# Kernel optimization log

Measured on AMD Instinct MI355X. Metric: run time of the kernel, lower is better.

## Reference

```python
import jax, jax.numpy as jnp
import numpy as np

NEG_INF = 1e20  # matches INF in the torch source
EPS = 1e-12     # F.normalize default eps
THRESHOLD = 0.1  # config.graph_learn_epsilon_label2label


def setup_inputs() -> dict:
    key = jax.random.key(0)
    k1, k2, k3, k4, k5 = jax.random.split(key, 5)
    L, E, E_PT, H = 2048, 512, 300, 16
    return {
        "label_embedding": jax.random.normal(k1, (L, E), dtype=jnp.float32),
        "pretrained_label_embedding": jax.random.normal(k2, (L, E_PT), dtype=jnp.float32),
        "W_pt": jax.random.normal(k3, (H, E_PT), dtype=jnp.float32) * 0.1,
        "W_gcn0": jax.random.normal(k4, (E, E), dtype=jnp.float32) * (1.0 / np.sqrt(E)),
        "W_gcn1": jax.random.normal(k5, (E, E), dtype=jnp.float32) * (1.0 / np.sqrt(E)),
    }


def _weighted_cosine(input_pt, W_pt):
    # W_pt: [H, E_pt]; input_pt: [L, E_pt]
    w2 = W_pt ** 2                                  # [H, E_pt]
    h = input_pt[None, :, :] * w2[:, None, :]       # [H, L, E_pt]
    norm = jnp.linalg.norm(h, axis=-1, keepdims=True)
    h_norm = h / jnp.maximum(norm, EPS)             # F.normalize(p=2, dim=-1)
    # mean over heads of per-head cosine similarity: [L, L]
    scores = jnp.einsum("hle,hme->hlm", h_norm, h_norm).mean(axis=0)
    return scores


def reference(label_embedding, pretrained_label_embedding, W_pt, W_gcn0, W_gcn1):
    # 1) metric-based graph structure learning
    scores_cosine = _weighted_cosine(pretrained_label_embedding, W_pt)
    scores = jnp.where(scores_cosine >= THRESHOLD, scores_cosine, -NEG_INF)
    adj = jax.nn.softmax(scores, axis=-1)           # [L, L]

    # 2) 2-layer GCN message passing (bias=None, batch_norm=False, eval-mode dropout)
    x = jax.nn.relu(adj @ (label_embedding @ W_gcn0))
    x = jax.nn.relu(adj @ (x @ W_gcn1))
    return x
```

## Files before the change

kernel.cpp:

```cpp
#include <hip/hip_runtime.h>
#include <hip/hip_bf16.h>


typedef __attribute__((ext_vector_type(8))) short bf16x8;
typedef __attribute__((ext_vector_type(4))) float f32x4;
typedef __attribute__((ext_vector_type(4))) int i32x4;

#define L_DIM 2048
#define EPT 300
#define H_DIM 16
#define KDIM 4800
#define WINDOW 1.5e-3f

__global__ __launch_bounds__(256) void prep_kernel(const float* __restrict__ xpt,
                                                   const float* __restrict__ Wpt,
                                                   const float* __restrict__ label,
                                                   const float* __restrict__ W0,
                                                   const float* __restrict__ W1,
                                                   signed char* __restrict__ Y,
                                                   float* __restrict__ rnorms,
                                                   float* __restrict__ inv_s,
                                                   __hip_bfloat16* __restrict__ Lbf,
                                                   __hip_bfloat16* __restrict__ W0t,
                                                   __hip_bfloat16* __restrict__ W1t) {
  __shared__ float redmax[4];
  __shared__ float tile[32][33];
  const int b = blockIdx.x;
  const int tid = threadIdx.x;
  if (b < 2048) {
    const int i = b;
    const int lane = tid & 63;
    const int w = tid >> 6;
    const float* x = xpt + i * EPT;
    float y[4][5];
    float wmax = 0.f;
#pragma unroll
    for (int hh = 0; hh < 4; ++hh) {
      const int h = w * 4 + hh;
      const float* wp = Wpt + h * EPT;
      float ss = 0.f;
#pragma unroll
      for (int t = 0; t < 5; ++t) {
        int e = lane + 64 * t;
        float val = 0.f;
        if (e < EPT) {
          float we = wp[e];
          val = x[e] * we * we;
        }
        y[hh][t] = val;
        ss += val * val;
      }
#pragma unroll
      for (int o = 32; o >= 1; o >>= 1) ss += __shfl_xor(ss, o, 64);
      float n = fmaxf(sqrtf(ss), 1e-12f);
      if (lane == 0) rnorms[i * H_DIM + h] = 1.0f / n;
      float scale = 0.25f / n;
#pragma unroll
      for (int t = 0; t < 5; ++t) {
        y[hh][t] *= scale;
        wmax = fmaxf(wmax, fabsf(y[hh][t]));
      }
    }
#pragma unroll
    for (int o = 32; o >= 1; o >>= 1) wmax = fmaxf(wmax, __shfl_xor(wmax, o, 64));
    if (lane == 0) redmax[w] = wmax;
    __syncthreads();
    float rowmax = fmaxf(fmaxf(redmax[0], redmax[1]), fmaxf(redmax[2], redmax[3]));
    rowmax = fmaxf(rowmax, 1e-12f);
    const float qs = 127.0f / rowmax;
    if (tid == 0) inv_s[i] = rowmax * (1.0f / 127.0f);
#pragma unroll
    for (int hh = 0; hh < 4; ++hh) {
      const int h = w * 4 + hh;
#pragma unroll
      for (int t = 0; t < 5; ++t) {
        int e = lane + 64 * t;
        if (e < EPT) {
          int qv = __float2int_rn(y[hh][t] * qs);
          qv = max(-127, min(127, qv));
          Y[(size_t)i * KDIM + h * EPT + e] = (signed char)qv;
        }
      }
    }
    return;
  }
  if (b < 6144) {
    int i = (b - 2048) * 256 + tid;
    Lbf[i] = __float2bfloat16(label[i]);
    return;
  }
  int local = b - 6144;
  const bool first = local < 256;
  const float* src = first ? W0 : W1;
  __hip_bfloat16* dst = first ? W0t : W1t;
  int rem = local & 255;
  int c0 = (rem & 15) * 32, r0 = (rem >> 4) * 32;
  int tx = tid & 31, ty = tid >> 5;
  for (int i2 = ty; i2 < 32; i2 += 8) tile[i2][tx] = src[(size_t)(r0 + i2) * 512 + c0 + tx];
  __syncthreads();
  for (int i2 = ty; i2 < 32; i2 += 8)
    dst[(size_t)(c0 + i2) * 512 + r0 + tx] = __float2bfloat16(tile[tx][i2]);
}

__global__ __launch_bounds__(256) void gram_i8(const signed char* __restrict__ Y,
                                               float* __restrict__ S,
                                               const float* __restrict__ inv_s,
                                               const __hip_bfloat16* __restrict__ W0t,
                                               const __hip_bfloat16* __restrict__ Lbf,
                                               __hip_bfloat16* __restrict__ T0t) {
  __shared__ __attribute__((aligned(16))) char smem[32768];
  const int id = blockIdx.x;
  const int bx = (id & 7) | (((id >> 3) & 3) << 3);
  const int by = id >> 5;
  const int row0 = by * 64, col0 = bx * 64;
  const int tid = threadIdx.x;
  const int lane = tid & 63;
  const int wn = tid >> 6;
  const int r = lane & 15, q = lane >> 4;

  if (col0 + 64 <= row0) {
    const int d = (by * (by - 1)) / 2 + bx;
    if (d >= 256) return;
    const int row0r = (d >> 5) * 64;
    const int col0r = (d & 31) * 64;
    __hip_bfloat16* Asb = (__hip_bfloat16*)smem;
    __hip_bfloat16* Bsb = (__hip_bfloat16*)(smem + 16384);
    const int srow8 = tid >> 3;
    const int schunk8 = (tid & 7) ^ (srow8 & 7);
    f32x4 racc[4];
#pragma unroll
    for (int t = 0; t < 4; ++t) {
      f32x4 z = {0.f, 0.f, 0.f, 0.f};
      racc[t] = z;
    }
#define RSTAGE(bufi, k0)                                                                      \
  {                                                                                           \
    _Pragma("unroll") for (int it = 0; it < 2; ++it) {                                        \
      __builtin_amdgcn_global_load_lds(                                                       \
          (const __attribute__((address_space(1))) void*)(W0t + (size_t)(row0r + it * 32 + srow8) * 512 + \
                                                          (k0) + schunk8 * 8),                \
          (__attribute__((address_space(3))) void*)(Asb + (bufi)*4096 + (it * 256 + tid) * 8), 16, 0, 0); \
    }                                                                                         \
    _Pragma("unroll") for (int it = 0; it < 2; ++it) {                                        \
      __builtin_amdgcn_global_load_lds(                                                       \
          (const __attribute__((address_space(1))) void*)(Lbf + (size_t)(col0r + it * 32 + srow8) * 512 + \
                                                          (k0) + schunk8 * 8),                \
          (__attribute__((address_space(3))) void*)(Bsb + (bufi)*4096 + (it * 256 + tid) * 8), 16, 0, 0); \
    }                                                                                         \
  }
    RSTAGE(0, 0)
    for (int k = 0; k < 8; ++k) {
      __syncthreads();
      if (k + 1 < 8) RSTAGE((k + 1) & 1, (k + 1) * 64)
      const __hip_bfloat16* as = Asb + (k & 1) * 4096;
      const __hip_bfloat16* bs = Bsb + (k & 1) * 4096;
#pragma unroll
      for (int kk = 0; kk < 2; ++kk) {
        const int ch = ((kk * 4 + q) ^ (r & 7)) * 8;
        bf16x8 af[4];
#pragma unroll
        for (int t = 0; t < 4; ++t) af[t] = *(const bf16x8*)(as + (t * 16 + r) * 64 + ch);
        bf16x8 bfr = *(const bf16x8*)(bs + (wn * 16 + r) * 64 + ch);
#pragma unroll
        for (int t = 0; t < 4; ++t)
          racc[t] = __builtin_amdgcn_mfma_f32_16x16x32_bf16(af[t], bfr, racc[t], 0, 0, 0);
      }
    }
#undef RSTAGE
    const int gcr = col0r + wn * 16 + r;
#pragma unroll
    for (int t = 0; t < 4; ++t) {
      int gr0 = row0r + t * 16 + q * 4;
#pragma unroll
      for (int p = 0; p < 4; ++p)
        T0t[(size_t)(gr0 + p) * 2048 + gcr] = __float2bfloat16(racc[t][p]);
    }
    return;
  }

  const bool do_mirror = (col0 > row0);
  signed char* As = (signed char*)smem;
  signed char* Bs = (signed char*)(smem + 16384);
  const int srow = tid >> 2;
  const int sc = (tid & 3) ^ ((srow >> 2) & 3);

  i32x4 acc[4];
#pragma unroll
  for (int t = 0; t < 4; ++t) {
    i32x4 z = {0, 0, 0, 0};
    acc[t] = z;
  }
  const int niter = KDIM / 64;

#define STAGEI(bufi, k0)                                                                       \
  {                                                                                            \
    __builtin_amdgcn_global_load_lds(                                                          \
        (const __attribute__((address_space(1))) void*)(Y + (size_t)(row0 + srow) * KDIM +     \
                                                        (k0) + sc * 16),                       \
        (__attribute__((address_space(3))) void*)(As + (bufi)*4096 + tid * 16), 16, 0, 0);     \
    __builtin_amdgcn_global_load_lds(                                                          \
        (const __attribute__((address_space(1))) void*)(Y + (size_t)(col0 + srow) * KDIM +     \
                                                        (k0) + sc * 16),                       \
        (__attribute__((address_space(3))) void*)(Bs + (bufi)*4096 + tid * 16), 16, 0, 0);     \
  }

  auto compute = [&](int bufi) {
    const signed char* as = As + bufi * 4096;
    const signed char* bs = Bs + bufi * 4096;
    const int ch = (q ^ ((r >> 2) & 3)) * 16;
    i32x4 bfrag = *(const i32x4*)(bs + (wn * 16 + r) * 64 + ch);
#pragma unroll
    for (int t = 0; t < 4; ++t) {
      i32x4 afrag = *(const i32x4*)(as + (t * 16 + r) * 64 + ch);
      acc[t] = __builtin_amdgcn_mfma_i32_16x16x64_i8(afrag, bfrag, acc[t], 0, 0, 0);
    }
  };

  STAGEI(0, 0)
  STAGEI(1, 64)
  STAGEI(2, 128)
  for (int k = 0; k < niter - 3; ++k) {
    asm volatile("s_waitcnt vmcnt(4)" ::: "memory");
    __builtin_amdgcn_s_barrier();
    __builtin_amdgcn_sched_barrier(0);
    STAGEI((k + 3) & 3, (k + 3) * 64)
    compute(k & 3);
  }
  asm volatile("s_waitcnt vmcnt(4)" ::: "memory");
  __builtin_amdgcn_s_barrier();
  __builtin_amdgcn_sched_barrier(0);
  compute((niter - 3) & 3);
  asm volatile("s_waitcnt vmcnt(2)" ::: "memory");
  __builtin_amdgcn_s_barrier();
  __builtin_amdgcn_sched_barrier(0);
  compute((niter - 2) & 3);
  asm volatile("s_waitcnt vmcnt(0)" ::: "memory");
  __builtin_amdgcn_s_barrier();
  __builtin_amdgcn_sched_barrier(0);
  compute((niter - 1) & 3);
#undef STAGEI
  const int gc = col0 + wn * 16 + r;
  const float sj = inv_s[gc];
#pragma unroll
  for (int t = 0; t < 4; ++t) {
    int gr0 = row0 + t * 16 + q * 4;
#pragma unroll
    for (int p = 0; p < 4; ++p) {
      float vv = (float)acc[t][p] * (inv_s[gr0 + p] * sj);
      S[(size_t)(gr0 + p) * L_DIM + gc] = vv;
      if (do_mirror) S[(size_t)gc * L_DIM + (gr0 + p)] = vv;
    }
  }
}

template <int BM, int BN, bool RELU, bool OUT_BF16>
__global__ __launch_bounds__(256) void gemm_bt(const __hip_bfloat16* __restrict__ A,
                                               const __hip_bfloat16* __restrict__ B,
                                               void* __restrict__ C0v,
                                               int M, int N, int K) {
  constexpr int WMG = BM / 64;
  constexpr int WNG = 4 / WMG;
  constexpr int NC = BN / (16 * WNG);
  const int row0 = blockIdx.y * BM, col0 = blockIdx.x * BN;
  __shared__ __attribute__((aligned(16))) __hip_bfloat16 As[2][BM * 64];
  __shared__ __attribute__((aligned(16))) __hip_bfloat16 Bs[2][BN * 64];
  const int tid = threadIdx.x;
  const int lane = tid & 63;
  const int wave = tid >> 6;
  const int wm = wave / WNG, wn = wave % WNG;
  const int r = lane & 15, q = lane >> 4;
  const int srow = tid >> 3;
  const int schunk = (tid & 7) ^ (srow & 7);

  f32x4 acc[4][NC];
#pragma unroll
  for (int a = 0; a < 4; ++a)
#pragma unroll
    for (int b = 0; b < NC; ++b) {
      f32x4 z = {0.f, 0.f, 0.f, 0.f};
      acc[a][b] = z;
    }

  const int niter = K >> 6;

#define STAGE(bufi, k0)                                                                       \
  {                                                                                           \
    _Pragma("unroll") for (int it = 0; it < BM / 32; ++it) {                                  \
      __builtin_amdgcn_global_load_lds(                                                       \
          (const __attribute__((address_space(1))) void*)(A + (size_t)(row0 + it * 32 + srow) * K + \
                                                          (k0) + schunk * 8),                 \
          (__attribute__((address_space(3))) void*)(&As[bufi][(it * 256 + tid) * 8]), 16, 0, 0); \
    }                                                                                         \
    _Pragma("unroll") for (int it = 0; it < BN / 32; ++it) {                                  \
      __builtin_amdgcn_global_load_lds(                                                       \
          (const __attribute__((address_space(1))) void*)(B + (size_t)(col0 + it * 32 + srow) * K + \
                                                          (k0) + schunk * 8),                 \
          (__attribute__((address_space(3))) void*)(&Bs[bufi][(it * 256 + tid) * 8]), 16, 0, 0); \
    }                                                                                         \
  }

  STAGE(0, 0)
  for (int k = 0; k < niter; ++k) {
    __syncthreads();
    if (k + 1 < niter) STAGE((k + 1) & 1, (k + 1) << 6)
    const __hip_bfloat16* as = As[k & 1];
    const __hip_bfloat16* bs = Bs[k & 1];
#pragma unroll
    for (int kk = 0; kk < 2; ++kk) {
      const int ch = ((kk * 4 + q) ^ (r & 7)) * 8;
      bf16x8 af[4], bfr[NC];
#pragma unroll
      for (int t = 0; t < 4; ++t)
        af[t] = *(const bf16x8*)(as + (wm * 64 + t * 16 + r) * 64 + ch);
#pragma unroll
      for (int c = 0; c < NC; ++c)
        bfr[c] = *(const bf16x8*)(bs + (wn * 16 * NC + c * 16 + r) * 64 + ch);
#pragma unroll
      for (int tm = 0; tm < 4; ++tm)
#pragma unroll
        for (int tn = 0; tn < NC; ++tn)
          acc[tm][tn] = __builtin_amdgcn_mfma_f32_16x16x32_bf16(af[tm], bfr[tn], acc[tm][tn], 0, 0, 0);
    }
  }
#undef STAGE
#pragma unroll
  for (int tm = 0; tm < 4; ++tm) {
    int gr0 = row0 + wm * 64 + tm * 16 + q * 4;
#pragma unroll
    for (int tn = 0; tn < NC; ++tn) {
      int gc = col0 + wn * 16 * NC + tn * 16 + r;
#pragma unroll
      for (int p = 0; p < 4; ++p) {
        float vv = acc[tm][tn][p];
        if (RELU) vv = fmaxf(vv, 0.f);
        if (OUT_BF16) {
          ((__hip_bfloat16*)C0v)[(size_t)(gr0 + p) * N + gc] = __float2bfloat16(vv);
        } else {
          ((float*)C0v)[(size_t)(gr0 + p) * N + gc] = vv;
        }
      }
    }
  }
}

template <bool OUT_BF16>
__global__ __launch_bounds__(512) void gemm_adj_fused(const __hip_bfloat16* __restrict__ A,
                                                      const __hip_bfloat16* __restrict__ B,
                                                      void* __restrict__ C0v) {
  constexpr int K = 2048, N = 512;
  __shared__ __attribute__((aligned(16))) __hip_bfloat16 sm[4][2][4096];
  const int tid = threadIdx.x;
  const int grp = tid >> 8;
  const int gtid = tid & 255;
  const int lane = tid & 63;
  const int wn = (tid >> 6) & 3;
  const int r = lane & 15, q = lane >> 4;
  const int srow = gtid >> 3;
  const int schunk = (gtid & 7) ^ (srow & 7);
  const int row0 = blockIdx.y * 64, col0 = blockIdx.x * 64;
  const int kbeg = grp * 1024;
  __hip_bfloat16* As = &sm[grp * 2 + 0][0][0];
  __hip_bfloat16* Bs = &sm[grp * 2 + 1][0][0];

  f32x4 acc[4];
#pragma unroll
  for (int t = 0; t < 4; ++t) {
    f32x4 z = {0.f, 0.f, 0.f, 0.f};
    acc[t] = z;
  }

#define FSTAGE(bufi, k0)                                                                      \
  {                                                                                           \
    _Pragma("unroll") for (int it = 0; it < 2; ++it) {                                        \
      __builtin_amdgcn_global_load_lds(                                                       \
          (const __attribute__((address_space(1))) void*)(A + (size_t)(row0 + it * 32 + srow) * K + \
                                                          (k0) + schunk * 8),                 \
          (__attribute__((address_space(3))) void*)(As + (bufi)*4096 + (it * 256 + gtid) * 8), 16, 0, 0); \
    }                                                                                         \
    _Pragma("unroll") for (int it = 0; it < 2; ++it) {                                        \
      __builtin_amdgcn_global_load_lds(                                                       \
          (const __attribute__((address_space(1))) void*)(B + (size_t)(col0 + it * 32 + srow) * K + \
                                                          (k0) + schunk * 8),                 \
          (__attribute__((address_space(3))) void*)(Bs + (bufi)*4096 + (it * 256 + gtid) * 8), 16, 0, 0); \
    }                                                                                         \
  }

  FSTAGE(0, kbeg)
  for (int k = 0; k < 16; ++k) {
    __syncthreads();
    if (k + 1 < 16) FSTAGE((k + 1) & 1, kbeg + ((k + 1) << 6))
    const __hip_bfloat16* as = As + (k & 1) * 4096;
    const __hip_bfloat16* bs = Bs + (k & 1) * 4096;
#pragma unroll
    for (int kk = 0; kk < 2; ++kk) {
      const int ch = ((kk * 4 + q) ^ (r & 7)) * 8;
      bf16x8 af[4];
#pragma unroll
      for (int t = 0; t < 4; ++t) af[t] = *(const bf16x8*)(as + (t * 16 + r) * 64 + ch);
      bf16x8 bfr = *(const bf16x8*)(bs + (wn * 16 + r) * 64 + ch);
#pragma unroll
      for (int t = 0; t < 4; ++t)
        acc[t] = __builtin_amdgcn_mfma_f32_16x16x32_bf16(af[t], bfr, acc[t], 0, 0, 0);
    }
  }
#undef FSTAGE
  __syncthreads();
  float* F = (float*)&sm[2][0][0];
  if (grp == 1) {
#pragma unroll
    for (int tm = 0; tm < 4; ++tm)
#pragma unroll
      for (int p = 0; p < 4; ++p) F[gtid * 16 + tm * 4 + p] = acc[tm][p];
  }
  __syncthreads();
  if (grp == 0) {
#pragma unroll
    for (int tm = 0; tm < 4; ++tm) {
      int gr0 = row0 + tm * 16 + q * 4;
      int gc = col0 + wn * 16 + r;
#pragma unroll
      for (int p = 0; p < 4; ++p) {
        float vv = fmaxf(acc[tm][p] + F[gtid * 16 + tm * 4 + p], 0.f);
        if (OUT_BF16) {
          ((__hip_bfloat16*)C0v)[(size_t)(gr0 + p) * N + gc] = __float2bfloat16(vv);
        } else {
          ((float*)C0v)[(size_t)(gr0 + p) * N + gc] = vv;
        }
      }
    }
  }
}

__global__ __launch_bounds__(256) void post_kernel(const float* __restrict__ S,
                                                   __hip_bfloat16* __restrict__ adj,
                                                   const float* __restrict__ xpt,
                                                   const float* __restrict__ Wpt,
                                                   const float* __restrict__ rnorms) {
  __shared__ float rowv[L_DIM];
  __shared__ int lq[1024];
  __shared__ int lcount;
  __shared__ float red[4];
  const int b = blockIdx.x;
  const int tid = threadIdx.x;
  if (tid == 0) lcount = 0;
  __syncthreads();
  const float* s = S + (size_t)b * L_DIM;
  for (int j0 = tid * 4; j0 < L_DIM; j0 += 1024) {
    float4 v = *(const float4*)(s + j0);
    *(float4*)(&rowv[j0]) = v;
    float vv[4] = {v.x, v.y, v.z, v.w};
#pragma unroll
    for (int u = 0; u < 4; ++u) {
      if (fabsf(vv[u] - 0.1f) < WINDOW) {
        int p = atomicAdd(&lcount, 1);
        if (p < 1024) lq[p] = j0 + u;
      }
    }
  }
  __syncthreads();
  const int n = min(lcount, 1024);
  if (n > 0) {
    const int lane = tid & 63;
    const int wave = tid >> 6;
    float xiv[5];
    float w4i[H_DIM][5];
    {
      const float* xi = xpt + b * EPT;
#pragma unroll
      for (int t = 0; t < 5; ++t) {
        int idx = lane + 64 * t;
        xiv[t] = idx < EPT ? xi[idx] : 0.f;
      }
#pragma unroll
      for (int h = 0; h < H_DIM; ++h) {
        float rni = rnorms[b * H_DIM + h];
#pragma unroll
        for (int t = 0; t < 5; ++t) {
          int idx = lane + 64 * t;
          float w = idx < EPT ? Wpt[h * EPT + idx] : 0.f;
          float w2 = w * w;
          w4i[h][t] = w2 * w2 * rni;
        }
      }
    }
    for (int k = wave; k < n; k += 4) {
      int j = lq[k];
      const float* xj = xpt + j * EPT;
      float pre[5];
#pragma unroll
      for (int t = 0; t < 5; ++t) {
        int idx = lane + 64 * t;
        pre[t] = idx < EPT ? xiv[t] * xj[idx] : 0.f;
      }
      float accv = 0.f;
#pragma unroll
      for (int h = 0; h < H_DIM; ++h) {
        float ph = 0.f;
#pragma unroll
        for (int t = 0; t < 5; ++t) ph += pre[t] * w4i[h][t];
        accv += ph * rnorms[j * H_DIM + h];
      }
#pragma unroll
      for (int o = 32; o >= 1; o >>= 1) accv += __shfl_xor(accv, o, 64);
      if (lane == 0) rowv[j] = accv * (1.f / 16.f);
    }
    __syncthreads();
  }
  float m = -1e30f;
  for (int j = tid; j < L_DIM; j += 256) {
    float v = rowv[j];
    if (v >= 0.1f && v > m) m = v;
  }
#pragma unroll
  for (int o = 32; o >= 1; o >>= 1) m = fmaxf(m, __shfl_xor(m, o, 64));
  if ((tid & 63) == 0) red[tid >> 6] = m;
  __syncthreads();
  m = fmaxf(fmaxf(red[0], red[1]), fmaxf(red[2], red[3]));
  float sum = 0.f;
  for (int j = tid; j < L_DIM; j += 256) {
    float v = rowv[j];
    if (v >= 0.1f) sum += __expf(v - m);
  }
#pragma unroll
  for (int o = 32; o >= 1; o >>= 1) sum += __shfl_xor(sum, o, 64);
  __syncthreads();
  if ((tid & 63) == 0) red[tid >> 6] = sum;
  __syncthreads();
  sum = red[0] + red[1] + red[2] + red[3];
  float inv = 1.f / sum;
  for (int j = tid; j < L_DIM; j += 256) {
    float v = rowv[j];
    float a = (v >= 0.1f) ? __expf(v - m) * inv : 0.f;
    adj[(size_t)b * L_DIM + j] = __float2bfloat16(a);
  }
}

extern "C" void kernel_launch(void* const* d_in, const int* in_sizes, int n_in, void* d_out,
                              int out_size, void* d_ws, size_t ws_size, hipStream_t stream) {
  const float* label = (const float*)d_in[0];
  const float* xpt = (const float*)d_in[1];
  const float* Wpt = (const float*)d_in[2];
  const float* W0 = (const float*)d_in[3];
  const float* W1 = (const float*)d_in[4];
  float* out = (float*)d_out;

  char* ws = (char*)d_ws;
  signed char* Y = (signed char*)ws;
  float* S = (float*)(ws + 19660800);
  float* rnorms = (float*)(ws + 36438016);
  float* inv_s = (float*)(ws + 44957696);
  __hip_bfloat16* Lbf = (__hip_bfloat16*)(ws + 44965888);
  __hip_bfloat16* adj = (__hip_bfloat16*)ws;
  __hip_bfloat16* W0t = (__hip_bfloat16*)(ws + 10485760);
  __hip_bfloat16* W1t = (__hip_bfloat16*)(ws + 11010048);
  __hip_bfloat16* T0t = (__hip_bfloat16*)(ws + 11534336);
  __hip_bfloat16* X1 = (__hip_bfloat16*)(ws + 13631488);
  __hip_bfloat16* T1t = (__hip_bfloat16*)(ws + 15728640);

  prep_kernel<<<6656, 256, 0, stream>>>(xpt, Wpt, label, W0, W1, Y, rnorms, inv_s, Lbf, W0t, W1t);
  gram_i8<<<1024, 256, 0, stream>>>(Y, S, inv_s, W0t, Lbf, T0t);
  post_kernel<<<2048, 256, 0, stream>>>(S, adj, xpt, Wpt, rnorms);
  gemm_adj_fused<true><<<dim3(8, 32), 512, 0, stream>>>(adj, T0t, X1);
  gemm_bt<64, 64, false, true><<<dim3(32, 8), 256, 0, stream>>>(W1t, X1, T1t, 512, 2048, 512);
  gemm_adj_fused<false><<<dim3(8, 32), 512, 0, stream>>>(adj, T1t, out);
}
```

Before: 180.9 us.

## Switch int8 Gram GEMM to 128-wide K tiles with double buffering

The int8 similarity GEMM main loop now stages 128-byte K slices per iteration in two LDS buffers instead of 64-byte slices in a four-deep ring. It uses an 8-way XOR swizzle and a 64-wide tail step for the leftover K. The aim is to halve the number of barrier and loop iterations and to issue two MFMAs per fragment load. In exchange the prefetch depth drops from three stages to one, and __syncthreads waits for all loads each iteration, which may expose memory latency.

```diff
diff --git a/kernel.cpp b/kernel.cpp
--- a/kernel.cpp
+++ b/kernel.cpp
@@ -181,8 +181,6 @@
   const bool do_mirror = (col0 > row0);
   signed char* As = (signed char*)smem;
   signed char* Bs = (signed char*)(smem + 16384);
-  const int srow = tid >> 2;
-  const int sc = (tid & 3) ^ ((srow >> 2) & 3);
 
   i32x4 acc[4];
 #pragma unroll
@@ -190,55 +188,79 @@
     i32x4 z = {0, 0, 0, 0};
     acc[t] = z;
   }
-  const int niter = KDIM / 64;
-
-#define STAGEI(bufi, k0)                                                                       \
+  constexpr int NF = 37;
+
+#define STAGE128(bufi, k0)                                                                     \
   {                                                                                            \
+    _Pragma("unroll") for (int it = 0; it < 2; ++it) {                                         \
+      const int idx = it * 256 + tid;                                                          \
+      const int srw = idx >> 3;                                                                \
+      const int scc = (idx & 7) ^ (srw & 7);                                                   \
+      __builtin_amdgcn_global_load_lds(                                                        \
+          (const __attribute__((address_space(1))) void*)(Y + (size_t)(row0 + srw) * KDIM +    \
+                                                          (k0) + scc * 16),                    \
+          (__attribute__((address_space(3))) void*)(As + (bufi)*8192 + idx * 16), 16, 0, 0);   \
+    }                                                                                          \
+    _Pragma("unroll") for (int it = 0; it < 2; ++it) {                                         \
+      const int idx = it * 256 + tid;                                                          \
+      const int srw = idx >> 3;                                                                \
+      const int scc = (idx & 7) ^ (srw & 7);                                                   \
+      __builtin_amdgcn_global_load_lds(                                                        \
+          (const __attribute__((address_space(1))) void*)(Y + (size_t)(col0 + srw) * KDIM +    \
+                                                          (k0) + scc * 16),                    \
+          (__attribute__((address_space(3))) void*)(Bs + (bufi)*8192 + idx * 16), 16, 0, 0);   \
+    }                                                                                          \
+  }
+
+#define STAGETAIL(bufi, k0)                                                                    \
+  {                                                                                            \
+    const int srw = tid >> 2;                                                                  \
+    const int scc = (tid & 3) ^ ((srw >> 2) & 3);                                              \
     __builtin_amdgcn_global_load_lds(                                                          \
-        (const __attribute__((address_space(1))) void*)(Y + (size_t)(row0 + srow) * KDIM +     \
-                                                        (k0) + sc * 16),                       \
-        (__attribute__((address_space(3))) void*)(As + (bufi)*4096 + tid * 16), 16, 0, 0);     \
+        (const __attribute__((address_space(1))) void*)(Y + (size_t)(row0 + srw) * KDIM +      \
+                                                        (k0) + scc * 16),                      \
+        (__attribute__((address_space(3))) void*)(As + (bufi)*8192 + tid * 16), 16, 0, 0);     \
     __builtin_amdgcn_global_load_lds(                                                          \
-        (const __attribute__((address_space(1))) void*)(Y + (size_t)(col0 + srow) * KDIM +     \
-                                                        (k0) + sc * 16),                       \
-        (__attribute__((address_space(3))) void*)(Bs + (bufi)*4096 + tid * 16), 16, 0, 0);     \
-  }
-
-  auto compute = [&](int bufi) {
-    const signed char* as = As + bufi * 4096;
-    const signed char* bs = Bs + bufi * 4096;
-    const int ch = (q ^ ((r >> 2) & 3)) * 16;
-    i32x4 bfrag = *(const i32x4*)(bs + (wn * 16 + r) * 64 + ch);
-#pragma unroll
-    for (int t = 0; t < 4; ++t) {
-      i32x4 afrag = *(const i32x4*)(as + (t * 16 + r) * 64 + ch);
-      acc[t] = __builtin_amdgcn_mfma_i32_16x16x64_i8(afrag, bfrag, acc[t], 0, 0, 0);
-    }
-  };
-
-  STAGEI(0, 0)
-  STAGEI(1, 64)
-  STAGEI(2, 128)
-  for (int k = 0; k < niter - 3; ++k) {
-    asm volatile("s_waitcnt vmcnt(4)" ::: "memory");
-    __builtin_amdgcn_s_barrier();
-    __builtin_amdgcn_sched_barrier(0);
-    STAGEI((k + 3) & 3, (k + 3) * 64)
-    compute(k & 3);
-  }
-  asm volatile("s_waitcnt vmcnt(4)" ::: "memory");
-  __builtin_amdgcn_s_barrier();
-  __builtin_amdgcn_sched_barrier(0);
-  compute((niter - 3) & 3);
-  asm volatile("s_waitcnt vmcnt(2)" ::: "memory");
-  __builtin_amdgcn_s_barrier();
-  __builtin_amdgcn_sched_barrier(0);
-  compute((niter - 2) & 3);
-  asm volatile("s_waitcnt vmcnt(0)" ::: "memory");
-  __builtin_amdgcn_s_barrier();
-  __builtin_amdgcn_sched_barrier(0);
-  compute((niter - 1) & 3);
-#undef STAGEI
+        (const __attribute__((address_space(1))) void*)(Y + (size_t)(col0 + srw) * KDIM +      \
+                                                        (k0) + scc * 16),                      \
+        (__attribute__((address_space(3))) void*)(Bs + (bufi)*8192 + tid * 16), 16, 0, 0);     \
+  }
+
+  STAGE128(0, 0)
+  for (int k = 0; k <= NF; ++k) {
+    __syncthreads();
+    if (k + 1 < NF) {
+      STAGE128((k + 1) & 1, (k + 1) * 128)
+    } else if (k + 1 == NF) {
+      STAGETAIL((k + 1) & 1, NF * 128)
+    }
+    if (k < NF) {
+      const signed char* as = As + (k & 1) * 8192;
+      const signed char* bs = Bs + (k & 1) * 8192;
+#pragma unroll
+      for (int kk = 0; kk < 2; ++kk) {
+        const int ch = ((kk * 4 + q) ^ (r & 7)) * 16;
+        i32x4 bfrag = *(const i32x4*)(bs + (wn * 16 + r) * 128 + ch);
+#pragma unroll
+        for (int t = 0; t < 4; ++t) {
+          i32x4 afrag = *(const i32x4*)(as + (t * 16 + r) * 128 + ch);
+          acc[t] = __builtin_amdgcn_mfma_i32_16x16x64_i8(afrag, bfrag, acc[t], 0, 0, 0);
+        }
+      }
+    } else {
+      const signed char* as = As + (k & 1) * 8192;
+      const signed char* bs = Bs + (k & 1) * 8192;
+      const int ch = (q ^ ((r >> 2) & 3)) * 16;
+      i32x4 bfrag = *(const i32x4*)(bs + (wn * 16 + r) * 64 + ch);
+#pragma unroll
+      for (int t = 0; t < 4; ++t) {
+        i32x4 afrag = *(const i32x4*)(as + (t * 16 + r) * 64 + ch);
+        acc[t] = __builtin_amdgcn_mfma_i32_16x16x64_i8(afrag, bfrag, acc[t], 0, 0, 0);
+      }
+    }
+  }
+#undef STAGE128
+#undef STAGETAIL
   const int gc = col0 + wn * 16 + r;
   const float sj = inv_s[gc];
 #pragma unroll
```

New measurement: 174.2 us (median of 2 runs). -3.7%, faster.
